# Optimization experiments

Measured on AMD Instinct MI355X. Metric: run time of the kernel, lower is better.

## Reference

```python
import jax, jax.numpy as jnp
import numpy as np

N_NODES = 50000
NEG_SLOPE = 0.2  # PyG GATConv default


def setup_inputs() -> dict:
    key = jax.random.key(0)
    ks = jax.random.split(key, 10)
    N, D_IN, HID, H, D_OUT, E = N_NODES, 256, 64, 4, 40, 800000
    inp = {
        "x": jax.random.normal(ks[0], (N, D_IN), jnp.float32),
        "edge_index": jax.random.randint(ks[1], (2, E), 0, N, jnp.int32),
        "W1": jax.random.normal(ks[2], (D_IN, H * HID), jnp.float32) * (1.0 / np.sqrt(D_IN)),
        "att_src1": jax.random.normal(ks[3], (H, HID), jnp.float32) * 0.1,
        "att_dst1": jax.random.normal(ks[4], (H, HID), jnp.float32) * 0.1,
        "b1": jnp.zeros((H * HID,), jnp.float32),
        "W2": jax.random.normal(ks[5], (H * HID, D_OUT), jnp.float32) * (1.0 / np.sqrt(H * HID)),
        "att_src2": jax.random.normal(ks[6], (1, D_OUT), jnp.float32) * 0.1,
        "att_dst2": jax.random.normal(ks[7], (1, D_OUT), jnp.float32) * 0.1,
        "b2": jnp.zeros((D_OUT,), jnp.float32),
    }
    return inp


def _gat_conv(x, src, dst, W, a_src, a_dst, b, n_nodes):
    """One GATConv layer (PyG semantics, self-loops already in src/dst)."""
    H, F = a_src.shape
    h = (x @ W).reshape(n_nodes, H, F)                      # [N,H,F]
    a_s = jnp.einsum('nhf,hf->nh', h, a_src)                # [N,H]
    a_d = jnp.einsum('nhf,hf->nh', h, a_dst)                # [N,H]
    e = jax.nn.leaky_relu(a_s[src] + a_d[dst], NEG_SLOPE)   # [E,H]
    # segment softmax over incoming edges of each destination node
    m = jax.ops.segment_max(e, dst, num_segments=n_nodes)   # [N,H]
    ex = jnp.exp(e - m[dst])                                # [E,H]
    den = jax.ops.segment_sum(ex, dst, num_segments=n_nodes)
    alpha = ex / den[dst]                                   # [E,H]
    out = jax.ops.segment_sum(h[src] * alpha[:, :, None], dst, num_segments=n_nodes)
    return out.reshape(n_nodes, H * F) + b


def reference(x, edge_index, W1, att_src1, att_dst1, b1, W2, att_src2, att_dst2, b2):
    N = x.shape[0]
    loop = jnp.arange(N, dtype=edge_index.dtype)
    src = jnp.concatenate([edge_index[0], loop])
    dst = jnp.concatenate([edge_index[1], loop])
    h = jax.nn.relu(_gat_conv(x, src, dst, W1, att_src1, att_dst1, b1, N))
    logits = _gat_conv(h, src, dst, W2, att_src2, att_dst2, b2, N)
    return jax.nn.log_softmax(logits, axis=1)
```

## Files before the change

### kernel.cpp

```cpp
#include <hip/hip_runtime.h>
#include <hip/hip_fp16.h>
#include <hip/hip_fp8.h>
#include <math.h>

#define NEG_SLOPE 0.2f

typedef short short8v __attribute__((ext_vector_type(8)));
typedef _Float16 half8v __attribute__((ext_vector_type(8)));
typedef float f32x4 __attribute__((ext_vector_type(4)));

__device__ __forceinline__ unsigned short f2bf(float f) {
    unsigned int u = __builtin_bit_cast(unsigned int, f);
    u += 0x7FFFu + ((u >> 16) & 1u);
    return (unsigned short)(u >> 16);
}

__device__ __forceinline__ unsigned char f2fp8(float f) {
    __hip_fp8_e4m3 q(f);
    return (unsigned char)q.__x;
}

__device__ __forceinline__ float fp82f(unsigned char b) {
    __hip_fp8_e4m3 q;
    q.__x = (__hip_fp8_storage_t)b;
    return (float)q;
}

__device__ __forceinline__ void fma_fp8x4(float4& acc, float w, unsigned v) {
    acc.x += w * fp82f((unsigned char)(v & 0xffu));
    acc.y += w * fp82f((unsigned char)((v >> 8) & 0xffu));
    acc.z += w * fp82f((unsigned char)((v >> 16) & 0xffu));
    acc.w += w * fp82f((unsigned char)(v >> 24));
}

__global__ void k_deg_cvt(const int* __restrict__ ei, int E, int N, int degB,
                          int* __restrict__ deg, int* __restrict__ rank,
                          const float* __restrict__ W1, const float* __restrict__ W2,
                          unsigned short* __restrict__ w1t, __half* __restrict__ w2t) {
    int b = blockIdx.x;
    if (b < degB) {
        int i = b * 256 + threadIdx.x;
        int Et = E + N;
        if (i >= Et) return;
        int dst = (i < E) ? ei[E + i] : (i - E);
        rank[i] = atomicAdd(&deg[dst], 1);
    } else {
        int bb = b - degB;
        int k = threadIdx.x;
        if (bb < 256) {
            w1t[bb * 256 + k] = f2bf(W1[k * 256 + bb]);
        } else {
            int c = bb - 256;
            w2t[c * 256 + k] = __float2half((c < 40) ? W2[k * 40 + c] : 0.f);
        }
    }
}

__global__ void k_scan_block(const int* __restrict__ deg, int N, int* __restrict__ excl, int* __restrict__ bsums) {
    __shared__ int s[256];
    int b = blockIdx.x, t = threadIdx.x;
    int i = b * 256 + t;
    int v = (i < N) ? deg[i] : 0;
    s[t] = v;
    __syncthreads();
    for (int off = 1; off < 256; off <<= 1) {
        int add = (t >= off) ? s[t - off] : 0;
        __syncthreads();
        s[t] += add;
        __syncthreads();
    }
    int incl = s[t];
    if (i < N) excl[i] = incl - v;
    if (t == 255) bsums[b] = incl;
}

__global__ void k_scan_add(int* __restrict__ row_start, const int* __restrict__ bsums,
                           int N, int Et, int NB) {
    __shared__ int ws[4];
    int b = blockIdx.x, t = threadIdx.x;
    int wv = t >> 6, l = t & 63;
    int v = (t < b && t < NB) ? bsums[t] : 0;
    for (int off = 32; off; off >>= 1) v += __shfl_xor(v, off);
    if (l == 0) ws[wv] = v;
    __syncthreads();
    int total = ws[0] + ws[1] + ws[2] + ws[3];
    int i = b * 256 + t;
    if (i < N) row_start[i] += total;
    if (i == 0) row_start[N] = Et;
}

__global__ void k_scatter(const int* __restrict__ ei, const int* __restrict__ rank, int E, int N,
                          const int* __restrict__ row_start, int* __restrict__ csr_src) {
    int i = blockIdx.x * blockDim.x + threadIdx.x;
    int Et = E + N;
    if (i >= Et) return;
    int src, dst;
    if (i < E) { src = ei[i]; dst = ei[E + i]; }
    else       { src = i - E; dst = i - E; }
    csr_src[row_start[dst] + rank[i]] = src;
}

#define LDP 264
__global__ __launch_bounds__(256) void k_gemm1_mfma(const float* __restrict__ x,
                                                    const unsigned short* __restrict__ w1t,
                                                    const float* __restrict__ att_s,
                                                    const float* __restrict__ att_d,
                                                    unsigned char* __restrict__ h1f,
                                                    float* __restrict__ as1, float* __restrict__ ad1, int N) {
    __shared__ unsigned short As[64 * LDP];
    __shared__ unsigned short Bs[64 * LDP];
    int tid = threadIdx.x;
    int row0 = blockIdx.x * 64;
#pragma unroll
    for (int it = 0; it < 16; it++) {
        int c = tid + it * 256;
        int r = c >> 6, q = c & 63;
        float4 v = make_float4(0, 0, 0, 0);
        if (row0 + r < N) v = ((const float4*)x)[(size_t)(row0 + r) * 64 + q];
        ushort4 o;
        o.x = f2bf(v.x); o.y = f2bf(v.y); o.z = f2bf(v.z); o.w = f2bf(v.w);
        *(ushort4*)&As[r * LDP + q * 4] = o;
    }
    int w = tid >> 6, l = tid & 63;
    int hi = l >> 4, lo = l & 15;
    short8v a[8];
    for (int head = 0; head < 4; head++) {
#pragma unroll
        for (int it = 0; it < 8; it++) {
            int c = tid + it * 256;
            int r = c >> 5, q = c & 31;
            uint4 vb = ((const uint4*)w1t)[(size_t)(head * 64 + r) * 32 + q];
            *(uint4*)&Bs[r * LDP + q * 8] = vb;
        }
        __syncthreads();
        if (head == 0) {
#pragma unroll
            for (int kk = 0; kk < 8; kk++)
                a[kk] = *(const short8v*)&As[(16 * w + lo) * LDP + kk * 32 + 8 * hi];
        }
        f32x4 acc[4] = {};
#pragma unroll
        for (int kk = 0; kk < 8; kk++) {
#pragma unroll
            for (int jb = 0; jb < 4; jb++) {
                short8v b = *(const short8v*)&Bs[(16 * jb + lo) * LDP + kk * 32 + 8 * hi];
                acc[jb] = __builtin_amdgcn_mfma_f32_16x16x32_bf16(a[kk], b, acc[jb], 0, 0, 0);
            }
        }
        float asr[4], adr[4];
#pragma unroll
        for (int jb = 0; jb < 4; jb++) {
            int c = head * 64 + lo + 16 * jb;
            asr[jb] = att_s[c];
            adr[jb] = att_d[c];
        }
#pragma unroll
        for (int j = 0; j < 4; j++) {
            int rr = 16 * w + 4 * hi + j;
            int r = row0 + rr;
            float s = 0.f, d = 0.f;
#pragma unroll
            for (int jb = 0; jb < 4; jb++) {
                float v = acc[jb][j];
                s += v * asr[jb];
                d += v * adr[jb];
                if (r < N) h1f[(size_t)r * 256 + head * 64 + lo + 16 * jb] = f2fp8(v);
            }
            s += __shfl_xor(s, 1); s += __shfl_xor(s, 2); s += __shfl_xor(s, 4); s += __shfl_xor(s, 8);
            d += __shfl_xor(d, 1); d += __shfl_xor(d, 2); d += __shfl_xor(d, 4); d += __shfl_xor(d, 8);
            if (lo == 0 && r < N) {
                as1[r * 4 + head] = s;
                ad1[r * 4 + head] = d;
            }
        }
        if (head < 3) __syncthreads();
    }
}

__global__ __launch_bounds__(256) void k_agg1(const unsigned char* __restrict__ h1f, const float* __restrict__ as1,
                                              const float* __restrict__ ad1, const int* __restrict__ row_start,
                                              const int* __restrict__ csr_src, const float* __restrict__ b1,
                                              __half* __restrict__ hbh, int N) {
    __shared__ int    s_src[4][64];
    __shared__ float4 s_w[4][64];
    int wv = threadIdx.x >> 6, l = threadIdx.x & 63;
    int n = blockIdx.x * 4 + wv;
    if (n >= N) return;
    int s0 = row_start[n], s1 = row_start[n + 1];
    int head = l >> 4;
    unsigned lb4 = (unsigned)l * 4u;
    const char* h1b = (const char*)h1f;
    float4 adv = ((const float4*)ad1)[n];
    float4 acc0 = make_float4(0, 0, 0, 0), acc1 = acc0, acc2 = acc0, acc3 = acc0;
    float den = 0.f;
    for (int c0 = s0; c0 < s1; c0 += 64) {
        int cl = min(64, s1 - c0);
        if (l < cl) {
            int si = csr_src[c0 + l];
            s_src[wv][l] = si;
            float4 a = ((const float4*)as1)[si];
            float4 e;
            e.x = a.x + adv.x; e.x = e.x > 0.f ? e.x : NEG_SLOPE * e.x; e.x = __expf(e.x);
            e.y = a.y + adv.y; e.y = e.y > 0.f ? e.y : NEG_SLOPE * e.y; e.y = __expf(e.y);
            e.z = a.z + adv.z; e.z = e.z > 0.f ? e.z : NEG_SLOPE * e.z; e.z = __expf(e.z);
            e.w = a.w + adv.w; e.w = e.w > 0.f ? e.w : NEG_SLOPE * e.w; e.w = __expf(e.w);
            s_w[wv][l] = e;
        }
        int p = 0;
        for (; p + 8 <= cl; p += 8) {
            int ss[8]; float ww[8]; unsigned vv[8];
#pragma unroll
            for (int i = 0; i < 8; i++) {
                ss[i] = s_src[wv][p + i];
                ww[i] = ((const float*)&s_w[wv][p + i])[head];
            }
#pragma unroll
            for (int i = 0; i < 8; i++)
                vv[i] = *(const unsigned*)(h1b + (unsigned)ss[i] * 256u + lb4);
#pragma unroll
            for (int i = 0; i < 8; i++) {
                den += ww[i];
                if ((i & 3) == 0) fma_fp8x4(acc0, ww[i], vv[i]);
                if ((i & 3) == 1) fma_fp8x4(acc1, ww[i], vv[i]);
                if ((i & 3) == 2) fma_fp8x4(acc2, ww[i], vv[i]);
                if ((i & 3) == 3) fma_fp8x4(acc3, ww[i], vv[i]);
            }
        }
        for (; p + 4 <= cl; p += 4) {
            int sA = s_src[wv][p],     sB = s_src[wv][p + 1];
            int sC = s_src[wv][p + 2], sD = s_src[wv][p + 3];
            float wA = ((const float*)&s_w[wv][p    ])[head];
            float wB = ((const float*)&s_w[wv][p + 1])[head];
            float wC = ((const float*)&s_w[wv][p + 2])[head];
            float wD = ((const float*)&s_w[wv][p + 3])[head];
            unsigned vA = *(const unsigned*)(h1b + (unsigned)sA * 256u + lb4);
            unsigned vB = *(const unsigned*)(h1b + (unsigned)sB * 256u + lb4);
            unsigned vC = *(const unsigned*)(h1b + (unsigned)sC * 256u + lb4);
            unsigned vD = *(const unsigned*)(h1b + (unsigned)sD * 256u + lb4);
            den += (wA + wB) + (wC + wD);
            fma_fp8x4(acc0, wA, vA); fma_fp8x4(acc1, wB, vB);
            fma_fp8x4(acc2, wC, vC); fma_fp8x4(acc3, wD, vD);
        }
        for (; p < cl; p++) {
            int s = s_src[wv][p];
            float wg = ((const float*)&s_w[wv][p])[head];
            unsigned v = *(const unsigned*)(h1b + (unsigned)s * 256u + lb4);
            den += wg;
            fma_fp8x4(acc0, wg, v);
        }
    }
    float4 acc;
    acc.x = (acc0.x + acc1.x) + (acc2.x + acc3.x);
    acc.y = (acc0.y + acc1.y) + (acc2.y + acc3.y);
    acc.z = (acc0.z + acc1.z) + (acc2.z + acc3.z);
    acc.w = (acc0.w + acc1.w) + (acc2.w + acc3.w);
    float inv = 1.f / den;
    float4 b = ((const float4*)b1)[l];
    float r0 = acc.x * inv + b.x; r0 = r0 > 0.f ? r0 : 0.f;
    float r1 = acc.y * inv + b.y; r1 = r1 > 0.f ? r1 : 0.f;
    float r2 = acc.z * inv + b.z; r2 = r2 > 0.f ? r2 : 0.f;
    float r3 = acc.w * inv + b.w; r3 = r3 > 0.f ? r3 : 0.f;
    unsigned short u0 = __builtin_bit_cast(unsigned short, __float2half(r0));
    unsigned short u1 = __builtin_bit_cast(unsigned short, __float2half(r1));
    unsigned short u2 = __builtin_bit_cast(unsigned short, __float2half(r2));
    unsigned short u3 = __builtin_bit_cast(unsigned short, __float2half(r3));
    uint2 st;
    st.x = (unsigned)u0 | ((unsigned)u1 << 16);
    st.y = (unsigned)u2 | ((unsigned)u3 << 16);
    *(uint2*)((char*)hbh + (unsigned)n * 512u + (unsigned)l * 8u) = st;
}

__global__ __launch_bounds__(256) void k_gemm2_mfma(const _Float16* __restrict__ hbh,
                                                    const _Float16* __restrict__ w2t,
                                                    const float* __restrict__ att_s2,
                                                    const float* __restrict__ att_d2,
                                                    __half* __restrict__ h2h,
                                                    float* __restrict__ as2, float* __restrict__ ad2, int N) {
    __shared__ _Float16 Hs[64 * LDP];
    __shared__ _Float16 Ws[48 * LDP];
    int tid = threadIdx.x;
    int row0 = blockIdx.x * 64;
#pragma unroll
    for (int it = 0; it < 8; it++) {
        int c = tid + it * 256;
        int r = c >> 5, q = c & 31;
        uint4 v = make_uint4(0, 0, 0, 0);
        if (row0 + r < N) v = ((const uint4*)hbh)[(size_t)(row0 + r) * 32 + q];
        *(uint4*)&Hs[r * LDP + q * 8] = v;
    }
#pragma unroll
    for (int it = 0; it < 6; it++) {
        int c = tid + it * 256;
        int r = c >> 5, q = c & 31;
        uint4 v = ((const uint4*)w2t)[c];
        *(uint4*)&Ws[r * LDP + q * 8] = v;
    }
    __syncthreads();
    int w = tid >> 6, l = tid & 63;
    int hi = l >> 4, lo = l & 15;
    f32x4 acc[3] = {};
#pragma unroll
    for (int kk = 0; kk < 8; kk++) {
        half8v a = *(const half8v*)&Hs[(16 * w + lo) * LDP + kk * 32 + 8 * hi];
#pragma unroll
        for (int jb = 0; jb < 3; jb++) {
            half8v b = *(const half8v*)&Ws[(16 * jb + lo) * LDP + kk * 32 + 8 * hi];
            acc[jb] = __builtin_amdgcn_mfma_f32_16x16x32_f16(a, b, acc[jb], 0, 0, 0);
        }
    }
    float asr[3], adr[3];
#pragma unroll
    for (int jb = 0; jb < 3; jb++) {
        int c = 16 * jb + lo;
        asr[jb] = (c < 40) ? att_s2[c] : 0.f;
        adr[jb] = (c < 40) ? att_d2[c] : 0.f;
    }
#pragma unroll
    for (int j = 0; j < 4; j++) {
        int r = row0 + 16 * w + 4 * hi + j;
        float s = 0.f, d = 0.f;
#pragma unroll
        for (int jb = 0; jb < 3; jb++) {
            float v = acc[jb][j];
            s += v * asr[jb];
            d += v * adr[jb];
            int c = 16 * jb + lo;
            if (c < 40 && r < N) h2h[(size_t)r * 40 + c] = __float2half(v);
        }
        s += __shfl_xor(s, 1); s += __shfl_xor(s, 2); s += __shfl_xor(s, 4); s += __shfl_xor(s, 8);
        d += __shfl_xor(d, 1); d += __shfl_xor(d, 2); d += __shfl_xor(d, 4); d += __shfl_xor(d, 8);
        if (lo == 0 && r < N) { as2[r] = s; ad2[r] = d; }
    }
}

__global__ __launch_bounds__(256) void k_agg2(const __half* __restrict__ h2h, const float* __restrict__ as2,
                                              const float* __restrict__ ad2, const int* __restrict__ row_start,
                                              const int* __restrict__ csr_src, const float* __restrict__ b2,
                                              float* __restrict__ out, int N) {
    __shared__ int   s_src[4][64];
    __shared__ float s_w[4][64];
    int wv = threadIdx.x >> 6, l = threadIdx.x & 63;
    int n = blockIdx.x * 4 + wv;
    if (n >= N) return;
    int s0 = row_start[n], s1 = row_start[n + 1];
    int grp = l / 20, li = l - grp * 20;
    unsigned li4 = (unsigned)li * 4u;
    const char* h2b = (const char*)h2h;
    float ad = ad2[n];
    float2 accA = make_float2(0.f, 0.f), accB = accA;
    float denA = 0.f, denB = 0.f;
    bool act = grp < 3;
    for (int c0 = s0; c0 < s1; c0 += 64) {
        int cl = min(64, s1 - c0);
        if (l < cl) {
            int si = csr_src[c0 + l];
            s_src[wv][l] = si;
            float e = as2[si] + ad;
            e = e > 0.f ? e : NEG_SLOPE * e;
            s_w[wv][l] = __expf(e);
        }
        if (act) {
            int p = grp;
            for (; p + 3 < cl; p += 6) {
                int sA = s_src[wv][p], sB = s_src[wv][p + 3];
                float wA = s_w[wv][p], wB = s_w[wv][p + 3];
                unsigned vA = *(const unsigned*)(h2b + (unsigned)sA * 80u + li4);
                unsigned vB = *(const unsigned*)(h2b + (unsigned)sB * 80u + li4);
                denA += wA; denB += wB;
                float2 fA = __half22float2(__builtin_bit_cast(__half2, vA));
                float2 fB = __half22float2(__builtin_bit_cast(__half2, vB));
                accA.x += wA * fA.x; accA.y += wA * fA.y;
                accB.x += wB * fB.x; accB.y += wB * fB.y;
            }
            for (; p < cl; p += 3) {
                int si = s_src[wv][p];
                float w = s_w[wv][p];
                unsigned v = *(const unsigned*)(h2b + (unsigned)si * 80u + li4);
                denA += w;
                float2 f = __half22float2(__builtin_bit_cast(__half2, v));
                accA.x += w * f.x; accA.y += w * f.y;
            }
        }
    }
    float den = denA + denB;
    float2 acc = make_float2(accA.x + accB.x, accA.y + accB.y);
    float den_t = __shfl(den, li) + __shfl(den, 20 + li) + __shfl(den, 40 + li);
    float ax = acc.x + __shfl(acc.x, l + 20) + __shfl(acc.x, l + 40);
    float ay = acc.y + __shfl(acc.y, l + 20) + __shfl(acc.y, l + 40);
    float inv = 1.f / den_t;
    float lg0 = -1e30f, lg1 = -1e30f;
    if (l < 20) {
        lg0 = ax * inv + b2[2 * l];
        lg1 = ay * inv + b2[2 * l + 1];
    }
    float mx = fmaxf(lg0, lg1);
    for (int off = 32; off; off >>= 1) mx = fmaxf(mx, __shfl_xor(mx, off));
    float s = (l < 20) ? (__expf(lg0 - mx) + __expf(lg1 - mx)) : 0.f;
    for (int off = 32; off; off >>= 1) s += __shfl_xor(s, off);
    float ls = logf(s);
    if (l < 20) {
        out[(size_t)n * 40 + 2 * l]     = lg0 - mx - ls;
        out[(size_t)n * 40 + 2 * l + 1] = lg1 - mx - ls;
    }
}

extern "C" void kernel_launch(void* const* d_in, const int* in_sizes, int n_in,
                              void* d_out, int out_size, void* d_ws, size_t ws_size,
                              hipStream_t stream) {
    const float* x      = (const float*)d_in[0];
    const int*   ei     = (const int*)d_in[1];
    const float* W1     = (const float*)d_in[2];
    const float* att_s1 = (const float*)d_in[3];
    const float* att_d1 = (const float*)d_in[4];
    const float* b1     = (const float*)d_in[5];
    const float* W2     = (const float*)d_in[6];
    const float* att_s2 = (const float*)d_in[7];
    const float* att_d2 = (const float*)d_in[8];
    const float* b2     = (const float*)d_in[9];

    int N = in_sizes[0] / 256;
    int E = in_sizes[1] / 2;
    int Et = E + N;

    char* ws = (char*)d_ws;
    size_t off = 0;
    auto alloc = [&](size_t bytes) -> void* {
        void* p = ws + off;
        off += (bytes + 255) / 256 * 256;
        return p;
    };
    unsigned char* h1f = (unsigned char*)alloc((size_t)N * 256);
    __half* hbh = (__half*)alloc((size_t)N * 256 * 2);
    __half* h2h = (__half*)alloc((size_t)N * 40 * 2);
    unsigned short* w1t = (unsigned short*)alloc((size_t)256 * 256 * 2);
    __half* w2t = (__half*)alloc((size_t)48 * 256 * 2);
    float* as1 = (float*)alloc((size_t)N * 4 * 4);
    float* ad1 = (float*)alloc((size_t)N * 4 * 4);
    float* as2 = (float*)alloc((size_t)N * 4);
    float* ad2 = (float*)alloc((size_t)N * 4);
    int* deg       = (int*)alloc((size_t)N * 4);
    int* rank      = (int*)alloc((size_t)Et * 4);
    int* row_start = (int*)alloc((size_t)(N + 1) * 4);
    int* csr_src   = (int*)alloc((size_t)Et * 4);
    int NB = (N + 255) / 256;
    int* bsums = (int*)alloc((size_t)NB * 4);

    hipMemsetAsync(deg, 0, (size_t)N * 4, stream);

    int degB = (Et + 255) / 256;
    k_deg_cvt<<<degB + 304, 256, 0, stream>>>(ei, E, N, degB, deg, rank, W1, W2, w1t, w2t);
    k_scan_block<<<NB, 256, 0, stream>>>(deg, N, row_start, bsums);
    k_scan_add<<<NB, 256, 0, stream>>>(row_start, bsums, N, Et, NB);
    k_scatter<<<degB, 256, 0, stream>>>(ei, rank, E, N, row_start, csr_src);

    k_gemm1_mfma<<<(N + 63) / 64, 256, 0, stream>>>(x, w1t, att_s1, att_d1, h1f, as1, ad1, N);
    k_agg1<<<(N + 3) / 4, 256, 0, stream>>>(h1f, as1, ad1, row_start, csr_src, b1, hbh, N);
    k_gemm2_mfma<<<(N + 63) / 64, 256, 0, stream>>>((const _Float16*)hbh, (const _Float16*)w2t,
                                                    att_s2, att_d2, h2h, as2, ad2, N);
    k_agg2<<<(N + 3) / 4, 256, 0, stream>>>(h2h, as2, ad2, row_start, csr_src, b2, (float*)d_out, N);
}
```

Baseline: 183.1 us.

## Share one LDS buffer in gemm1 and prefetch next head's weights into registers

After: 202.5 us. 10.6% more time.

```diff
diff --git a/kernel.cpp b/kernel.cpp
--- a/kernel.cpp
+++ b/kernel.cpp
@@ -101,14 +101,13 @@
 }
 
 #define LDP 264
-__global__ __launch_bounds__(256) void k_gemm1_mfma(const float* __restrict__ x,
-                                                    const unsigned short* __restrict__ w1t,
-                                                    const float* __restrict__ att_s,
-                                                    const float* __restrict__ att_d,
-                                                    unsigned char* __restrict__ h1f,
-                                                    float* __restrict__ as1, float* __restrict__ ad1, int N) {
-    __shared__ unsigned short As[64 * LDP];
-    __shared__ unsigned short Bs[64 * LDP];
+__global__ __launch_bounds__(256, 4) void k_gemm1_mfma(const float* __restrict__ x,
+                                                       const unsigned short* __restrict__ w1t,
+                                                       const float* __restrict__ att_s,
+                                                       const float* __restrict__ att_d,
+                                                       unsigned char* __restrict__ h1f,
+                                                       float* __restrict__ as1, float* __restrict__ ad1, int N) {
+    __shared__ unsigned short Sb[64 * LDP];
     int tid = threadIdx.x;
     int row0 = blockIdx.x * 64;
 #pragma unroll
@@ -119,31 +118,39 @@
         if (row0 + r < N) v = ((const float4*)x)[(size_t)(row0 + r) * 64 + q];
         ushort4 o;
         o.x = f2bf(v.x); o.y = f2bf(v.y); o.z = f2bf(v.z); o.w = f2bf(v.w);
-        *(ushort4*)&As[r * LDP + q * 4] = o;
-    }
+        *(ushort4*)&Sb[r * LDP + q * 4] = o;
+    }
+    __syncthreads();
     int w = tid >> 6, l = tid & 63;
     int hi = l >> 4, lo = l & 15;
     short8v a[8];
+#pragma unroll
+    for (int kk = 0; kk < 8; kk++)
+        a[kk] = *(const short8v*)&Sb[(16 * w + lo) * LDP + kk * 32 + 8 * hi];
+    uint4 vb[8];
+#pragma unroll
+    for (int it = 0; it < 8; it++) vb[it] = ((const uint4*)w1t)[tid + it * 256];
+    __syncthreads();
+#pragma unroll
+    for (int it = 0; it < 8; it++) {
+        int c = tid + it * 256;
+        int r = c >> 5, q = c & 31;
+        *(uint4*)&Sb[r * LDP + q * 8] = vb[it];
+    }
+    __syncthreads();
     for (int head = 0; head < 4; head++) {
-#pragma unroll
-        for (int it = 0; it < 8; it++) {
-            int c = tid + it * 256;
-            int r = c >> 5, q = c & 31;
-            uint4 vb = ((const uint4*)w1t)[(size_t)(head * 64 + r) * 32 + q];
-            *(uint4*)&Bs[r * LDP + q * 8] = vb;
-        }
-        __syncthreads();
-        if (head == 0) {
-#pragma unroll
-            for (int kk = 0; kk < 8; kk++)
-                a[kk] = *(const short8v*)&As[(16 * w + lo) * LDP + kk * 32 + 8 * hi];
+        uint4 nb[8];
+        if (head < 3) {
+#pragma unroll
+            for (int it = 0; it < 8; it++)
+                nb[it] = ((const uint4*)w1t)[(head + 1) * 2048 + tid + it * 256];
         }
         f32x4 acc[4] = {};
 #pragma unroll
         for (int kk = 0; kk < 8; kk++) {
 #pragma unroll
             for (int jb = 0; jb < 4; jb++) {
-                short8v b = *(const short8v*)&Bs[(16 * jb + lo) * LDP + kk * 32 + 8 * hi];
+                short8v b = *(const short8v*)&Sb[(16 * jb + lo) * LDP + kk * 32 + 8 * hi];
                 acc[jb] = __builtin_amdgcn_mfma_f32_16x16x32_bf16(a[kk], b, acc[jb], 0, 0, 0);
             }
         }
@@ -173,7 +180,16 @@
                 ad1[r * 4 + head] = d;
             }
         }
-        if (head < 3) __syncthreads();
+        if (head < 3) {
+            __syncthreads();
+#pragma unroll
+            for (int it = 0; it < 8; it++) {
+                int c = tid + it * 256;
+                int r = c >> 5, q = c & 31;
+                *(uint4*)&Sb[r * LDP + q * 8] = nb[it];
+            }
+            __syncthreads();
+        }
     }
 }
 
```
